# Optimization experiments

Hardware: AMD Instinct MI355X
Metric: run time of the kernel (lower is better)

The kernel has to match this reference:

```python
import jax, jax.numpy as jnp
import numpy as np

H = 2048          # hidden_size
F = 1408          # moe_intermediate_size
E = 64            # n_routed_experts
TOP_K = 6         # num_experts_per_tok
CAP = 512         # per-expert capacity (mean load ~192; overflow prob ~0)
SCALE = 1.0       # routed_scaling_factor
F_SH = 2 * F      # shared-expert intermediate (n_shared_experts=2)
B, S = 1, 2048


def setup_inputs() -> dict:
    key = jax.random.key(0)
    ks = jax.random.split(key, 8)
    s = 0.02
    return {
        "hidden_states": jax.random.normal(ks[0], (B, S, H), jnp.float32),
        "gate_w":  jax.random.normal(ks[1], (E, H), jnp.float32) * s,
        "w_gate":  jax.random.normal(ks[2], (E, H, F), jnp.float32) * s,
        "w_up":    jax.random.normal(ks[3], (E, H, F), jnp.float32) * s,
        "w_down":  jax.random.normal(ks[4], (E, F, H), jnp.float32) * s,
        "sh_gate": jax.random.normal(ks[5], (F_SH, H), jnp.float32) * s,
        "sh_up":   jax.random.normal(ks[6], (F_SH, H), jnp.float32) * s,
        "sh_down": jax.random.normal(ks[7], (H, F_SH), jnp.float32) * s,
    }


def reference(hidden_states, gate_w, w_gate, w_up, w_down, sh_gate, sh_up, sh_down):
    b, s, _ = hidden_states.shape
    x = hidden_states.reshape(-1, H)                       # [T, H]
    T = x.shape[0]

    # ---- gate: fp32 logits -> softmax -> top-k, scaled ----
    logits = x.astype(jnp.float32) @ gate_w.astype(jnp.float32).T   # [T, E]
    scores = jax.nn.softmax(logits, axis=-1)
    topk_w, topk_idx = jax.lax.top_k(scores, TOP_K)        # [T, K] (order irrelevant: summed)
    topk_w = topk_w * SCALE

    # ---- dispatch: sort expanded tokens by expert, scatter into [E, CAP, H] ----
    eid = topk_idx.reshape(-1)                             # [T*K]
    x_exp = jnp.repeat(x, TOP_K, axis=0)                   # [T*K, H] (token t repeated K times)
    order = jnp.argsort(eid)                               # stable sort by expert id
    eid_s = eid[order]
    counts = jnp.bincount(eid, length=E)
    starts = jnp.cumsum(counts) - counts                   # exclusive prefix sums
    pos = jnp.arange(T * TOP_K) - starts[eid_s]            # slot within expert
    valid = pos < CAP
    pos_c = jnp.where(valid, pos, CAP)                     # overflow -> scratch slot CAP
    buf = jnp.zeros((E, CAP + 1, H), x.dtype).at[eid_s, pos_c].set(x_exp[order])

    # ---- grouped expert SwiGLU MLP (grouped GEMM as batched einsum) ----
    g = jax.nn.silu(jnp.einsum('ech,ehf->ecf', buf, w_gate))
    u = jnp.einsum('ech,ehf->ecf', buf, w_up)
    d = jnp.einsum('ecf,efh->ech', g * u, w_down)          # [E, CAP+1, H]

    # ---- combine: gather, unsort, weighted sum over top-k ----
    out_s = jnp.where(valid[:, None], d[eid_s, pos_c], 0.0)
    out_exp = jnp.zeros_like(out_s).at[order].set(out_s)   # reverse_shuffle
    y = jnp.einsum('tkh,tk->th', out_exp.reshape(T, TOP_K, H), topk_w)
    y = y.astype(x.dtype).reshape(b, s, H)

    # ---- shared experts residual (dense SwiGLU MLP on identity) ----
    gs = jax.nn.silu(hidden_states @ sh_gate.T)
    us = hidden_states @ sh_up.T
    y = y + (gs * us) @ sh_down.T
    return y
```

## Files before the change

kernel.cpp:

```cpp
#include <hip/hip_runtime.h>
#include <hip/hip_bf16.h>

#define H 2048
#define FDIM 1408
#define NE 64
#define CAP 512
#define NTOK 2048
#define FSH 2816

typedef float  f32x4  __attribute__((ext_vector_type(4)));
typedef short  s16x8  __attribute__((ext_vector_type(8)));
typedef unsigned short u16;
typedef u16    u16x4v __attribute__((ext_vector_type(4)));

__device__ __forceinline__ u16 f2bf(float f) {
    union { float f; unsigned u; } v; v.f = f;
    unsigned u = v.u;
    u += 0x7fffu + ((u >> 16) & 1u);
    return (u16)(u >> 16);
}
__device__ __forceinline__ float bf2f(u16 b) {
    union { unsigned u; float f; } v; v.u = ((unsigned)b) << 16;
    return v.f;
}

#define BAR() do { asm volatile("s_waitcnt lgkmcnt(0)" ::: "memory"); \
                   __builtin_amdgcn_s_barrier(); } while (0)

__global__ __launch_bounds__(256) void xcvt(const float* __restrict__ x, u16* __restrict__ xb) {
    int i = blockIdx.x * 256 + threadIdx.x;
    const float4 a = ((const float4*)x)[2 * i];
    const float4 b = ((const float4*)x)[2 * i + 1];
    u16 v[8] = { f2bf(a.x), f2bf(a.y), f2bf(a.z), f2bf(a.w),
                 f2bf(b.x), f2bf(b.y), f2bf(b.z), f2bf(b.w) };
    *(s16x8*)(xb + (size_t)i * 8) = *(s16x8*)v;
}

__global__ void init_cnt(int* __restrict__ c) { c[threadIdx.x] = 0; }

__global__ __launch_bounds__(64) void gate_topk(
    const float* __restrict__ xg, const float* __restrict__ gw,
    int* __restrict__ cnt, int* __restrict__ tok_of,
    int* __restrict__ slot_enc, float* __restrict__ tw)
{
    const int t = blockIdx.x;
    const int lane = threadIdx.x;
    __shared__ float4 xs[512];
    const float4* xr = (const float4*)(xg + (size_t)t * H);
    #pragma unroll
    for (int i = 0; i < 8; ++i) xs[i * 64 + lane] = xr[i * 64 + lane];
    __syncthreads();

    const float4* gr = (const float4*)(gw + (size_t)lane * H);
    float acc = 0.f;
    #pragma unroll 4
    for (int i = 0; i < 512; ++i) {
        float4 a = xs[i], b = gr[i];
        acc += a.x * b.x + a.y * b.y + a.z * b.z + a.w * b.w;
    }
    float m = acc;
    #pragma unroll
    for (int off = 32; off; off >>= 1) m = fmaxf(m, __shfl_xor(m, off));
    float p = __expf(acc - m);
    float s = p;
    #pragma unroll
    for (int off = 32; off; off >>= 1) s += __shfl_xor(s, off);
    p = p / s;

    float myw = 0.f; int mye = 0;
    float v = p;
    for (int k = 0; k < 6; ++k) {
        float bv = v; int bi = lane;
        #pragma unroll
        for (int off = 32; off; off >>= 1) {
            float ov = __shfl_xor(bv, off);
            int   oi = __shfl_xor(bi, off);
            if (ov > bv || (ov == bv && oi < bi)) { bv = ov; bi = oi; }
        }
        if (lane == k)  { myw = bv; mye = bi; }
        if (lane == bi) v = -1.f;
    }
    if (lane < 6) {
        int slot = atomicAdd(&cnt[mye], 1);
        int enc = -1;
        if (slot < CAP) { tok_of[mye * CAP + slot] = t; enc = mye * CAP + slot; }
        slot_enc[t * 6 + lane] = enc;
        tw[t * 6 + lane] = myw;
    }
}

template<bool ROUTED>
__global__ __launch_bounds__(256, 2) void dual_gemm(
    const u16* __restrict__ xbf, const int* __restrict__ tok_of,
    const int* __restrict__ cnt_arr, const float* __restrict__ wg,
    const float* __restrict__ wu, u16* __restrict__ act, int Fd)
{
    __shared__ u16 As[2][8][256][8];
    __shared__ u16 Bs[2][2][8][32][8];

    int e = 0, cnt, m0, f0;
    if constexpr (ROUTED) {
        e = blockIdx.z;
        cnt = cnt_arr[e]; cnt = cnt < CAP ? cnt : CAP;
        f0 = blockIdx.x * 32; m0 = blockIdx.y * 256;
        if (m0 >= cnt) return;
    } else {
        cnt = NTOK;
        m0 = blockIdx.x * 256; f0 = blockIdx.y * 32;
    }

    const float* wg_e = wg;
    const float* wu_e = wu;
    u16* act_e = act;
    if constexpr (ROUTED) {
        wg_e += (size_t)e * H * Fd;
        wu_e += (size_t)e * H * Fd;
        act_e += (size_t)e * CAP * Fd;
    }

    const int tid = threadIdx.x;
    const int lane = tid & 63;
    const int wv = tid >> 6;

    const u16* aptr;
    {
        int srow = m0 + tid;
        if constexpr (ROUTED) {
            const int* tok = tok_of + e * CAP;
            aptr = xbf + (size_t)tok[srow < cnt ? srow : 0] * H;
        } else {
            aptr = xbf + (size_t)srow * H;
        }
    }
    const int mat = tid >> 7;
    const int bb = tid & 127;
    const float* bsrc;
    int n4 = 0, kq = 0, br = 0, bc = 0;
    if constexpr (ROUTED) {
        n4 = bb & 7; kq = bb >> 3;
        bsrc = (mat ? wu_e : wg_e) + (size_t)(kq * 4) * Fd + f0 + n4 * 4;
    } else {
        br = bb >> 2; bc = bb & 3;
        bsrc = (mat ? wu_e : wg_e) + (size_t)(f0 + br) * H + bc * 16;
    }

    s16x8 aR[8];
    f32x4 bR[4];
    f32x4 accg[4][2], accu[4][2];
    const f32x4 zero4 = {0.f, 0.f, 0.f, 0.f};
    #pragma unroll
    for (int i = 0; i < 4; ++i)
        #pragma unroll
        for (int j = 0; j < 2; ++j) { accg[i][j] = zero4; accu[i][j] = zero4; }

    auto LOAD = [&](int kt) {
        #pragma unroll
        for (int q = 0; q < 8; ++q) aR[q] = *(const s16x8*)(aptr + kt * 64 + q * 8);
        if constexpr (ROUTED) {
            #pragma unroll
            for (int j = 0; j < 4; ++j)
                bR[j] = *(const f32x4*)(bsrc + ((size_t)kt * 64 + j) * Fd);
        } else {
            #pragma unroll
            for (int q = 0; q < 4; ++q)
                bR[q] = *(const f32x4*)(bsrc + kt * 64 + q * 4);
        }
    };
    auto STORE = [&](int b) {
        #pragma unroll
        for (int q = 0; q < 8; ++q) *(s16x8*)&As[b][q][tid][0] = aR[q];
        if constexpr (ROUTED) {
            const int k8 = kq >> 1, ko = (kq & 1) * 4;
            #pragma unroll
            for (int c = 0; c < 4; ++c) {
                u16x4v v; v[0] = f2bf(bR[0][c]); v[1] = f2bf(bR[1][c]);
                          v[2] = f2bf(bR[2][c]); v[3] = f2bf(bR[3][c]);
                *(u16x4v*)&Bs[b][mat][k8][(n4 * 4 + c) ^ k8][ko] = v;
            }
        } else {
            #pragma unroll
            for (int h = 0; h < 2; ++h) {
                const int k8 = bc * 2 + h;
                u16 v[8];
                f32x4 x0 = bR[h * 2], x1 = bR[h * 2 + 1];
                v[0]=f2bf(x0[0]); v[1]=f2bf(x0[1]); v[2]=f2bf(x0[2]); v[3]=f2bf(x0[3]);
                v[4]=f2bf(x1[0]); v[5]=f2bf(x1[1]); v[6]=f2bf(x1[2]); v[7]=f2bf(x1[3]);
                *(s16x8*)&Bs[b][mat][k8][br ^ k8][0] = *(s16x8*)v;
            }
        }
    };

    LOAD(0); STORE(0); LOAD(1);
    BAR();
    for (int kt = 0; kt < H / 64; ++kt) {
        const int b = kt & 1;
        if (kt + 1 < H / 64) STORE(b ^ 1);
        if (kt + 2 < H / 64) LOAD(kt + 2);
        __builtin_amdgcn_s_setprio(1);
        #pragma unroll
        for (int kk = 0; kk < 2; ++kk) {
            const int k8 = kk * 4 + (lane >> 4);
            s16x8 a[4], bg[2], bu[2];
            #pragma unroll
            for (int mi = 0; mi < 4; ++mi)
                a[mi] = *(const s16x8*)&As[b][k8][wv * 64 + mi * 16 + (lane & 15)][0];
            #pragma unroll
            for (int ni = 0; ni < 2; ++ni) {
                const int np = (ni * 16 + (lane & 15)) ^ k8;
                bg[ni] = *(const s16x8*)&Bs[b][0][k8][np][0];
                bu[ni] = *(const s16x8*)&Bs[b][1][k8][np][0];
            }
            #pragma unroll
            for (int mi = 0; mi < 4; ++mi)
                #pragma unroll
                for (int ni = 0; ni < 2; ++ni) {
                    accg[mi][ni] = __builtin_amdgcn_mfma_f32_16x16x32_bf16(a[mi], bg[ni], accg[mi][ni], 0, 0, 0);
                    accu[mi][ni] = __builtin_amdgcn_mfma_f32_16x16x32_bf16(a[mi], bu[ni], accu[mi][ni], 0, 0, 0);
                }
        }
        __builtin_amdgcn_s_setprio(0);
        BAR();
    }

    #pragma unroll
    for (int mi = 0; mi < 4; ++mi)
        #pragma unroll
        for (int ni = 0; ni < 2; ++ni)
            #pragma unroll
            for (int r = 0; r < 4; ++r) {
                int srow = m0 + wv * 64 + mi * 16 + (lane >> 4) * 4 + r;
                if (srow < cnt) {
                    int fc = f0 + ni * 16 + (lane & 15);
                    float g = accg[mi][ni][r], u = accu[mi][ni][r];
                    float aa = (g / (1.f + __expf(-g))) * u;
                    act_e[(size_t)srow * Fd + fc] = f2bf(aa);
                }
            }
}

template<bool ROUTED>
__global__ __launch_bounds__(256, 2) void down_gemm(
    const u16* __restrict__ actA, const float* __restrict__ wdn,
    void* __restrict__ outp, const int* __restrict__ cnt_arr, int Kd)
{
    __shared__ u16 As[2][8][256][8];
    __shared__ u16 Bs[2][8][64][8];

    int e = 0, cnt, m0, n0;
    if constexpr (ROUTED) {
        e = blockIdx.z;
        cnt = cnt_arr[e]; cnt = cnt < CAP ? cnt : CAP;
        n0 = blockIdx.x * 64; m0 = blockIdx.y * 256;
        if (m0 >= cnt) return;
    } else {
        cnt = NTOK;
        m0 = blockIdx.x * 256; n0 = blockIdx.y * 64;
    }

    const u16* A_e = actA;
    const float* B_e = wdn;
    if constexpr (ROUTED) {
        A_e += (size_t)e * CAP * Kd;
        B_e += (size_t)e * Kd * H;
    }
    const int NT = Kd / 64;
    const int tid = threadIdx.x, lane = tid & 63, wv = tid >> 6;

    const u16* aptr;
    {
        int row = m0 + tid;
        if constexpr (ROUTED) aptr = A_e + (size_t)(row < cnt ? row : m0) * Kd;
        else aptr = A_e + (size_t)row * Kd;
    }
    const float* bsrc;
    int n4 = 0, kq = 0, br = 0, bc = 0;
    if constexpr (ROUTED) {
        n4 = tid & 15; kq = tid >> 4;
        bsrc = B_e + (size_t)(kq * 4) * H + n0 + n4 * 4;
    } else {
        br = tid >> 2; bc = tid & 3;
        bsrc = B_e + (size_t)(n0 + br) * FSH + bc * 16;
    }

    s16x8 aR[8];
    f32x4 bR[4];
    f32x4 acc[4][4];
    const f32x4 zero4 = {0.f, 0.f, 0.f, 0.f};
    #pragma unroll
    for (int i = 0; i < 4; ++i)
        #pragma unroll
        for (int j = 0; j < 4; ++j) acc[i][j] = zero4;

    auto LOAD = [&](int kt) {
        #pragma unroll
        for (int q = 0; q < 8; ++q) aR[q] = *(const s16x8*)(aptr + kt * 64 + q * 8);
        if constexpr (ROUTED) {
            #pragma unroll
            for (int j = 0; j < 4; ++j)
                bR[j] = *(const f32x4*)(bsrc + ((size_t)kt * 64 + j) * H);
        } else {
            #pragma unroll
            for (int q = 0; q < 4; ++q)
                bR[q] = *(const f32x4*)(bsrc + kt * 64 + q * 4);
        }
    };
    auto STORE = [&](int b) {
        #pragma unroll
        for (int q = 0; q < 8; ++q) *(s16x8*)&As[b][q][tid][0] = aR[q];
        if constexpr (ROUTED) {
            const int k8 = kq >> 1, ko = (kq & 1) * 4;
            #pragma unroll
            for (int c = 0; c < 4; ++c) {
                u16x4v v; v[0] = f2bf(bR[0][c]); v[1] = f2bf(bR[1][c]);
                          v[2] = f2bf(bR[2][c]); v[3] = f2bf(bR[3][c]);
                *(u16x4v*)&Bs[b][k8][(n4 * 4 + c) ^ k8][ko] = v;
            }
        } else {
            #pragma unroll
            for (int h = 0; h < 2; ++h) {
                const int k8 = bc * 2 + h;
                u16 v[8];
                f32x4 x0 = bR[h * 2], x1 = bR[h * 2 + 1];
                v[0]=f2bf(x0[0]); v[1]=f2bf(x0[1]); v[2]=f2bf(x0[2]); v[3]=f2bf(x0[3]);
                v[4]=f2bf(x1[0]); v[5]=f2bf(x1[1]); v[6]=f2bf(x1[2]); v[7]=f2bf(x1[3]);
                *(s16x8*)&Bs[b][k8][br ^ k8][0] = *(s16x8*)v;
            }
        }
    };

    LOAD(0); STORE(0); LOAD(1);
    BAR();
    for (int kt = 0; kt < NT; ++kt) {
        const int b = kt & 1;
        if (kt + 1 < NT) STORE(b ^ 1);
        if (kt + 2 < NT) LOAD(kt + 2);
        __builtin_amdgcn_s_setprio(1);
        #pragma unroll
        for (int kk = 0; kk < 2; ++kk) {
            const int k8 = kk * 4 + (lane >> 4);
            s16x8 a[4], bf[4];
            #pragma unroll
            for (int mi = 0; mi < 4; ++mi)
                a[mi] = *(const s16x8*)&As[b][k8][wv * 64 + mi * 16 + (lane & 15)][0];
            #pragma unroll
            for (int ni = 0; ni < 4; ++ni)
                bf[ni] = *(const s16x8*)&Bs[b][k8][(ni * 16 + (lane & 15)) ^ k8][0];
            #pragma unroll
            for (int mi = 0; mi < 4; ++mi)
                #pragma unroll
                for (int ni = 0; ni < 4; ++ni)
                    acc[mi][ni] = __builtin_amdgcn_mfma_f32_16x16x32_bf16(a[mi], bf[ni], acc[mi][ni], 0, 0, 0);
        }
        __builtin_amdgcn_s_setprio(0);
        BAR();
    }

    #pragma unroll
    for (int mi = 0; mi < 4; ++mi)
        #pragma unroll
        for (int ni = 0; ni < 4; ++ni)
            #pragma unroll
            for (int r = 0; r < 4; ++r) {
                int srow = m0 + wv * 64 + mi * 16 + (lane >> 4) * 4 + r;
                if (srow < cnt) {
                    int col = n0 + ni * 16 + (lane & 15);
                    float vv = acc[mi][ni][r];
                    if constexpr (ROUTED)
                        ((u16*)outp)[(size_t)e * CAP * H + (size_t)srow * H + col] = f2bf(vv);
                    else
                        ((float*)outp)[(size_t)srow * H + col] = vv;
                }
            }
}

__global__ __launch_bounds__(256) void combine(
    float* __restrict__ y, const u16* __restrict__ d,
    const int* __restrict__ slot_enc, const float* __restrict__ tw)
{
    const int t = blockIdx.x, tid = threadIdx.x;
    int enc[6]; float w[6];
    #pragma unroll
    for (int k = 0; k < 6; ++k) {
        enc[k] = slot_enc[t * 6 + k];
        w[k] = tw[t * 6 + k];
    }
    float4* yrow = (float4*)(y + (size_t)t * H);
    #pragma unroll
    for (int it = 0; it < 2; ++it) {
        int h4 = it * 256 + tid;
        float4 acc = yrow[h4];
        #pragma unroll
        for (int k = 0; k < 6; ++k) {
            if (enc[k] >= 0) {
                ushort4 dv = ((const ushort4*)(d + (size_t)enc[k] * H))[h4];
                acc.x += w[k] * bf2f(dv.x);
                acc.y += w[k] * bf2f(dv.y);
                acc.z += w[k] * bf2f(dv.z);
                acc.w += w[k] * bf2f(dv.w);
            }
        }
        yrow[h4] = acc;
    }
}

extern "C" void kernel_launch(void* const* d_in, const int* in_sizes, int n_in,
                              void* d_out, int out_size, void* d_ws, size_t ws_size,
                              hipStream_t stream) {
    const float* x       = (const float*)d_in[0];
    const float* gw      = (const float*)d_in[1];
    const float* w_gate  = (const float*)d_in[2];
    const float* w_up    = (const float*)d_in[3];
    const float* w_down  = (const float*)d_in[4];
    const float* sh_gate = (const float*)d_in[5];
    const float* sh_up   = (const float*)d_in[6];
    const float* sh_down = (const float*)d_in[7];
    float* y = (float*)d_out;

    char* wsb = (char*)d_ws;
    int*   cnt      = (int*)(wsb + 0);
    int*   tok_of   = (int*)(wsb + 512);
    int*   slot_enc = (int*)(wsb + 512 + 131072);
    float* tw       = (float*)(wsb + 512 + 131072 + 49152);
    u16*   act      = (u16*)(wsb + 230144);
    u16*   actsh    = (u16*)(wsb + 230144 + 92274688);
    u16*   dbuf     = (u16*)(wsb + 230144 + 92274688 + 11534336);
    u16*   xbf      = dbuf;

    init_cnt<<<1, 64, 0, stream>>>(cnt);
    xcvt<<<NTOK * H / 8 / 256, 256, 0, stream>>>(x, xbf);
    gate_topk<<<NTOK, 64, 0, stream>>>(x, gw, cnt, tok_of, slot_enc, tw);
    dual_gemm<true><<<dim3(FDIM / 32, 2, NE), 256, 0, stream>>>(
        xbf, tok_of, cnt, w_gate, w_up, act, FDIM);
    dual_gemm<false><<<dim3(NTOK / 256, FSH / 32, 1), 256, 0, stream>>>(
        xbf, nullptr, nullptr, sh_gate, sh_up, actsh, FSH);
    down_gemm<true><<<dim3(H / 64, 2, NE), 256, 0, stream>>>(
        act, w_down, (void*)dbuf, cnt, FDIM);
    down_gemm<false><<<dim3(NTOK / 256, H / 64, 1), 256, 0, stream>>>(
        actsh, sh_down, (void*)y, nullptr, FSH);
    combine<<<NTOK, 256, 0, stream>>>(y, dbuf, slot_enc, tw);
}
```

Baseline: 1.107 ms.

## Load A tiles straight into LDS and double-buffer B weight registers

In both the gate/up and down-projection GEMM kernels, the bf16 A tile is now copied from global memory directly into LDS with global_load_lds, so it no longer passes through VGPRs and explicit LDS stores. The fp32 B weights are held in two alternating register buffers. They are converted and written to LDS after the MFMA block, and explicit vmcnt waits plus scheduling fences control the overlap. The goal is to cut register pressure and VALU/LDS store traffic and to hide global latency behind compute. The risks are that the hand-counted vmcnt values must match the issue order exactly, and that the down kernel now reads unclamped padding rows of the expert buffer.

Result: slower. 1.465 ms (+32.4%).

```diff
diff --git a/kernel.cpp b/kernel.cpp
--- a/kernel.cpp
+++ b/kernel.cpp
@@ -23,9 +23,15 @@
     union { unsigned u; float f; } v; v.u = ((unsigned)b) << 16;
     return v.f;
 }
-
-#define BAR() do { asm volatile("s_waitcnt lgkmcnt(0)" ::: "memory"); \
-                   __builtin_amdgcn_s_barrier(); } while (0)
+__device__ __forceinline__ void glds16(const u16* g, u16* l) {
+    __builtin_amdgcn_global_load_lds(
+        (const __attribute__((address_space(1))) unsigned int*)g,
+        (__attribute__((address_space(3))) unsigned int*)l, 16, 0, 0);
+}
+
+#define WAIT_VM(N)  asm volatile("s_waitcnt vmcnt(" #N ")" ::: "memory")
+#define WAIT_LGKM() asm volatile("s_waitcnt lgkmcnt(0)" ::: "memory")
+#define SCHED_FENCE() __builtin_amdgcn_sched_barrier(0)
 
 __global__ __launch_bounds__(256) void xcvt(const float* __restrict__ x, u16* __restrict__ xb) {
     int i = blockIdx.x * 256 + threadIdx.x;
@@ -121,6 +127,7 @@
     const int tid = threadIdx.x;
     const int lane = tid & 63;
     const int wv = tid >> 6;
+    const int NT = H / 64;
 
     const u16* aptr;
     {
@@ -144,8 +151,7 @@
         bsrc = (mat ? wu_e : wg_e) + (size_t)(f0 + br) * H + bc * 16;
     }
 
-    s16x8 aR[8];
-    f32x4 bR[4];
+    f32x4 bRa[4], bRb[4];
     f32x4 accg[4][2], accu[4][2];
     const f32x4 zero4 = {0.f, 0.f, 0.f, 0.f};
     #pragma unroll
@@ -153,28 +159,29 @@
         #pragma unroll
         for (int j = 0; j < 2; ++j) { accg[i][j] = zero4; accu[i][j] = zero4; }
 
-    auto LOAD = [&](int kt) {
-        #pragma unroll
-        for (int q = 0; q < 8; ++q) aR[q] = *(const s16x8*)(aptr + kt * 64 + q * 8);
+    auto GLDS_A = [&](int kt, int b) {
+        #pragma unroll
+        for (int q = 0; q < 8; ++q)
+            glds16(aptr + kt * 64 + q * 8, &As[b][q][wv * 64][0]);
+    };
+    auto LOADB = [&](int kt, f32x4 (&dst)[4]) {
         if constexpr (ROUTED) {
             #pragma unroll
             for (int j = 0; j < 4; ++j)
-                bR[j] = *(const f32x4*)(bsrc + ((size_t)kt * 64 + j) * Fd);
+                dst[j] = *(const f32x4*)(bsrc + ((size_t)kt * 64 + j) * Fd);
         } else {
             #pragma unroll
             for (int q = 0; q < 4; ++q)
-                bR[q] = *(const f32x4*)(bsrc + kt * 64 + q * 4);
-        }
-    };
-    auto STORE = [&](int b) {
-        #pragma unroll
-        for (int q = 0; q < 8; ++q) *(s16x8*)&As[b][q][tid][0] = aR[q];
+                dst[q] = *(const f32x4*)(bsrc + kt * 64 + q * 4);
+        }
+    };
+    auto STOREB = [&](const f32x4 (&src)[4], int b) {
         if constexpr (ROUTED) {
             const int k8 = kq >> 1, ko = (kq & 1) * 4;
             #pragma unroll
             for (int c = 0; c < 4; ++c) {
-                u16x4v v; v[0] = f2bf(bR[0][c]); v[1] = f2bf(bR[1][c]);
-                          v[2] = f2bf(bR[2][c]); v[3] = f2bf(bR[3][c]);
+                u16x4v v; v[0] = f2bf(src[0][c]); v[1] = f2bf(src[1][c]);
+                          v[2] = f2bf(src[2][c]); v[3] = f2bf(src[3][c]);
                 *(u16x4v*)&Bs[b][mat][k8][(n4 * 4 + c) ^ k8][ko] = v;
             }
         } else {
@@ -182,20 +189,14 @@
             for (int h = 0; h < 2; ++h) {
                 const int k8 = bc * 2 + h;
                 u16 v[8];
-                f32x4 x0 = bR[h * 2], x1 = bR[h * 2 + 1];
+                f32x4 x0 = src[h * 2], x1 = src[h * 2 + 1];
                 v[0]=f2bf(x0[0]); v[1]=f2bf(x0[1]); v[2]=f2bf(x0[2]); v[3]=f2bf(x0[3]);
                 v[4]=f2bf(x1[0]); v[5]=f2bf(x1[1]); v[6]=f2bf(x1[2]); v[7]=f2bf(x1[3]);
                 *(s16x8*)&Bs[b][mat][k8][br ^ k8][0] = *(s16x8*)v;
             }
         }
     };
-
-    LOAD(0); STORE(0); LOAD(1);
-    BAR();
-    for (int kt = 0; kt < H / 64; ++kt) {
-        const int b = kt & 1;
-        if (kt + 1 < H / 64) STORE(b ^ 1);
-        if (kt + 2 < H / 64) LOAD(kt + 2);
+    auto COMPUTE = [&](int b) {
         __builtin_amdgcn_s_setprio(1);
         #pragma unroll
         for (int kk = 0; kk < 2; ++kk) {
@@ -219,7 +220,33 @@
                 }
         }
         __builtin_amdgcn_s_setprio(0);
-        BAR();
+    };
+
+    GLDS_A(0, 0);            SCHED_FENCE();
+    LOADB(0, bRa);           SCHED_FENCE();
+    LOADB(1, bRb);           SCHED_FENCE();
+    WAIT_VM(4);
+    STOREB(bRa, 0);
+    WAIT_LGKM();
+    __builtin_amdgcn_s_barrier();
+    SCHED_FENCE();
+
+    for (int kt = 0; kt < NT; ++kt) {
+        const int b = kt & 1;
+        if (kt + 1 < NT) GLDS_A(kt + 1, b ^ 1);
+        SCHED_FENCE();
+        if ((kt & 1) == 0) { if (kt + 2 < NT) LOADB(kt + 2, bRa); }
+        else               { if (kt + 2 < NT) LOADB(kt + 2, bRb); }
+        SCHED_FENCE();
+        COMPUTE(b);
+        if (kt + 1 < NT) {
+            if ((kt & 1) == 0) STOREB(bRb, b ^ 1);
+            else               STOREB(bRa, b ^ 1);
+        }
+        if (kt + 2 < NT) { WAIT_VM(4); } else { WAIT_VM(0); }
+        WAIT_LGKM();
+        __builtin_amdgcn_s_barrier();
+        SCHED_FENCE();
     }
 
     #pragma unroll
@@ -266,24 +293,19 @@
     const int NT = Kd / 64;
     const int tid = threadIdx.x, lane = tid & 63, wv = tid >> 6;
 
-    const u16* aptr;
-    {
-        int row = m0 + tid;
-        if constexpr (ROUTED) aptr = A_e + (size_t)(row < cnt ? row : m0) * Kd;
-        else aptr = A_e + (size_t)row * Kd;
-    }
+    const u16* aptr = A_e + (size_t)(m0 + tid) * Kd;
+
     const float* bsrc;
-    int n4 = 0, kq = 0, br = 0, bc = 0;
+    int n4 = 0, kq = 0, dr = 0, dc = 0;
     if constexpr (ROUTED) {
         n4 = tid & 15; kq = tid >> 4;
         bsrc = B_e + (size_t)(kq * 4) * H + n0 + n4 * 4;
     } else {
-        br = tid >> 2; bc = tid & 3;
-        bsrc = B_e + (size_t)(n0 + br) * FSH + bc * 16;
-    }
-
-    s16x8 aR[8];
-    f32x4 bR[4];
+        dr = tid >> 2; dc = tid & 3;
+        bsrc = B_e + (size_t)(n0 + dr) * FSH + dc * 16;
+    }
+
+    f32x4 bRa[4], bRb[4];
     f32x4 acc[4][4];
     const f32x4 zero4 = {0.f, 0.f, 0.f, 0.f};
     #pragma unroll
@@ -291,49 +313,44 @@
         #pragma unroll
         for (int j = 0; j < 4; ++j) acc[i][j] = zero4;
 
-    auto LOAD = [&](int kt) {
-        #pragma unroll
-        for (int q = 0; q < 8; ++q) aR[q] = *(const s16x8*)(aptr + kt * 64 + q * 8);
+    auto GLDS_A = [&](int kt, int b) {
+        #pragma unroll
+        for (int q = 0; q < 8; ++q)
+            glds16(aptr + kt * 64 + q * 8, &As[b][q][wv * 64][0]);
+    };
+    auto LOADB = [&](int kt, f32x4 (&dst)[4]) {
         if constexpr (ROUTED) {
             #pragma unroll
             for (int j = 0; j < 4; ++j)
-                bR[j] = *(const f32x4*)(bsrc + ((size_t)kt * 64 + j) * H);
+                dst[j] = *(const f32x4*)(bsrc + ((size_t)kt * 64 + j) * H);
         } else {
             #pragma unroll
             for (int q = 0; q < 4; ++q)
-                bR[q] = *(const f32x4*)(bsrc + kt * 64 + q * 4);
-        }
-    };
-    auto STORE = [&](int b) {
-        #pragma unroll
-        for (int q = 0; q < 8; ++q) *(s16x8*)&As[b][q][tid][0] = aR[q];
+                dst[q] = *(const f32x4*)(bsrc + kt * 64 + q * 4);
+        }
+    };
+    auto STOREB = [&](const f32x4 (&src)[4], int b) {
         if constexpr (ROUTED) {
             const int k8 = kq >> 1, ko = (kq & 1) * 4;
             #pragma unroll
             for (int c = 0; c < 4; ++c) {
-                u16x4v v; v[0] = f2bf(bR[0][c]); v[1] = f2bf(bR[1][c]);
-                          v[2] = f2bf(bR[2][c]); v[3] = f2bf(bR[3][c]);
+                u16x4v v; v[0] = f2bf(src[0][c]); v[1] = f2bf(src[1][c]);
+                          v[2] = f2bf(src[2][c]); v[3] = f2bf(src[3][c]);
                 *(u16x4v*)&Bs[b][k8][(n4 * 4 + c) ^ k8][ko] = v;
             }
         } else {
             #pragma unroll
             for (int h = 0; h < 2; ++h) {
-                const int k8 = bc * 2 + h;
+                const int k8 = dc * 2 + h;
                 u16 v[8];
-                f32x4 x0 = bR[h * 2], x1 = bR[h * 2 + 1];
+                f32x4 x0 = src[h * 2], x1 = src[h * 2 + 1];
                 v[0]=f2bf(x0[0]); v[1]=f2bf(x0[1]); v[2]=f2bf(x0[2]); v[3]=f2bf(x0[3]);
                 v[4]=f2bf(x1[0]); v[5]=f2bf(x1[1]); v[6]=f2bf(x1[2]); v[7]=f2bf(x1[3]);
-                *(s16x8*)&Bs[b][k8][br ^ k8][0] = *(s16x8*)v;
-            }
-        }
-    };
-
-    LOAD(0); STORE(0); LOAD(1);
-    BAR();
-    for (int kt = 0; kt < NT; ++kt) {
-        const int b = kt & 1;
-        if (kt + 1 < NT) STORE(b ^ 1);
-        if (kt + 2 < NT) LOAD(kt + 2);
+                *(s16x8*)&Bs[b][k8][dr ^ k8][0] = *(s16x8*)v;
+            }
+        }
+    };
+    auto COMPUTE = [&](int b) {
         __builtin_amdgcn_s_setprio(1);
         #pragma unroll
         for (int kk = 0; kk < 2; ++kk) {
@@ -352,7 +369,33 @@
                     acc[mi][ni] = __builtin_amdgcn_mfma_f32_16x16x32_bf16(a[mi], bf[ni], acc[mi][ni], 0, 0, 0);
         }
         __builtin_amdgcn_s_setprio(0);
-        BAR();
+    };
+
+    GLDS_A(0, 0);            SCHED_FENCE();
+    LOADB(0, bRa);           SCHED_FENCE();
+    LOADB(1, bRb);           SCHED_FENCE();
+    WAIT_VM(4);
+    STOREB(bRa, 0);
+    WAIT_LGKM();
+    __builtin_amdgcn_s_barrier();
+    SCHED_FENCE();
+
+    for (int kt = 0; kt < NT; ++kt) {
+        const int b = kt & 1;
+        if (kt + 1 < NT) GLDS_A(kt + 1, b ^ 1);
+        SCHED_FENCE();
+        if ((kt & 1) == 0) { if (kt + 2 < NT) LOADB(kt + 2, bRa); }
+        else               { if (kt + 2 < NT) LOADB(kt + 2, bRb); }
+        SCHED_FENCE();
+        COMPUTE(b);
+        if (kt + 1 < NT) {
+            if ((kt & 1) == 0) STOREB(bRb, b ^ 1);
+            else               STOREB(bRa, b ^ 1);
+        }
+        if (kt + 2 < NT) { WAIT_VM(4); } else { WAIT_VM(0); }
+        WAIT_LGKM();
+        __builtin_amdgcn_s_barrier();
+        SCHED_FENCE();
     }
 
     #pragma unroll
```

## Deepen GEMM prefetch to two register stages with XOR-swizzled LDS tiles

Applied to the files above, without the earlier changes.

Both the dual gate/up GEMM and the down GEMM now keep two register sets of global loads in flight. The k-loop is unrolled by two so that tile kt+3 is loaded while tile kt is computed, and scheduling fences keep the compiler from reordering across these stages. The LDS layout changes from a k8-major layout to row-major 64-wide rows with an XOR swizzle, and A-tile loads now read coalesced row chunks with eight rows per thread. This is meant to hide global-memory latency and cut LDS bank conflicts, at the cost of more registers, which may hurt occupancy under launch_bounds(256,2).

New measurement: 1.328 ms. 20.0% more time.

```diff
diff --git a/kernel.cpp b/kernel.cpp
--- a/kernel.cpp
+++ b/kernel.cpp
@@ -23,9 +23,17 @@
     union { unsigned u; float f; } v; v.u = ((unsigned)b) << 16;
     return v.f;
 }
+__device__ __forceinline__ int swze(int row) {
+    return (((row & 7) ^ ((row >> 3) & 7)) << 3);
+}
+__device__ __forceinline__ void wr4(u16* dst, float a, float b, float c, float d) {
+    u16x4v v; v[0] = f2bf(a); v[1] = f2bf(b); v[2] = f2bf(c); v[3] = f2bf(d);
+    *(u16x4v*)dst = v;
+}
 
 #define BAR() do { asm volatile("s_waitcnt lgkmcnt(0)" ::: "memory"); \
                    __builtin_amdgcn_s_barrier(); } while (0)
+#define SCHED_FENCE() __builtin_amdgcn_sched_barrier(0)
 
 __global__ __launch_bounds__(256) void xcvt(const float* __restrict__ x, u16* __restrict__ xb) {
     int i = blockIdx.x * 256 + threadIdx.x;
@@ -95,8 +103,9 @@
     const int* __restrict__ cnt_arr, const float* __restrict__ wg,
     const float* __restrict__ wu, u16* __restrict__ act, int Fd)
 {
-    __shared__ u16 As[2][8][256][8];
-    __shared__ u16 Bs[2][2][8][32][8];
+    __shared__ u16 As[2][256 * 64];
+    __shared__ u16 Bgs[2][32 * 64];
+    __shared__ u16 Bus[2][32 * 64];
 
     int e = 0, cnt, m0, f0;
     if constexpr (ROUTED) {
@@ -121,31 +130,35 @@
     const int tid = threadIdx.x;
     const int lane = tid & 63;
     const int wv = tid >> 6;
-
-    const u16* aptr;
-    {
-        int srow = m0 + tid;
+    const int NT = H / 64;
+
+    const int ac = tid & 7;
+    int arl[8];
+    const u16* arow[8];
+    #pragma unroll
+    for (int it = 0; it < 8; ++it) {
+        int row = it * 32 + (tid >> 3);
+        arl[it] = row;
+        int srow = m0 + row;
         if constexpr (ROUTED) {
             const int* tok = tok_of + e * CAP;
-            aptr = xbf + (size_t)tok[srow < cnt ? srow : 0] * H;
+            arow[it] = xbf + (size_t)tok[srow < cnt ? srow : 0] * H;
         } else {
-            aptr = xbf + (size_t)srow * H;
+            arow[it] = xbf + (size_t)srow * H;
         }
     }
     const int mat = tid >> 7;
     const int bb = tid & 127;
     const float* bsrc;
-    int n4 = 0, kq = 0, br = 0, bc = 0;
-    if constexpr (ROUTED) {
-        n4 = bb & 7; kq = bb >> 3;
-        bsrc = (mat ? wu_e : wg_e) + (size_t)(kq * 4) * Fd + f0 + n4 * 4;
+    int bn4 = 0, bkb = 0, br = 0, bc = 0;
+    if constexpr (ROUTED) {
+        bn4 = bb & 7; bkb = bb >> 3;
+        bsrc = (mat ? wu_e : wg_e) + (size_t)(bkb * 4) * Fd + f0 + bn4 * 4;
     } else {
         br = bb >> 2; bc = bb & 3;
         bsrc = (mat ? wu_e : wg_e) + (size_t)(f0 + br) * H + bc * 16;
     }
 
-    s16x8 aR[8];
-    f32x4 bR[4];
     f32x4 accg[4][2], accu[4][2];
     const f32x4 zero4 = {0.f, 0.f, 0.f, 0.f};
     #pragma unroll
@@ -153,62 +166,60 @@
         #pragma unroll
         for (int j = 0; j < 2; ++j) { accg[i][j] = zero4; accu[i][j] = zero4; }
 
-    auto LOAD = [&](int kt) {
-        #pragma unroll
-        for (int q = 0; q < 8; ++q) aR[q] = *(const s16x8*)(aptr + kt * 64 + q * 8);
+    s16x8 aR0[8], aR1[8];
+    f32x4 bR0[4], bR1[4];
+
+    auto LOADA = [&](int kt, s16x8 (&ar)[8]) {
+        #pragma unroll
+        for (int it = 0; it < 8; ++it)
+            ar[it] = *(const s16x8*)(arow[it] + kt * 64 + ac * 8);
+    };
+    auto LOADB = [&](int kt, f32x4 (&brg)[4]) {
         if constexpr (ROUTED) {
             #pragma unroll
             for (int j = 0; j < 4; ++j)
-                bR[j] = *(const f32x4*)(bsrc + ((size_t)kt * 64 + j) * Fd);
+                brg[j] = *(const f32x4*)(bsrc + ((size_t)kt * 64 + j) * Fd);
         } else {
             #pragma unroll
             for (int q = 0; q < 4; ++q)
-                bR[q] = *(const f32x4*)(bsrc + kt * 64 + q * 4);
-        }
-    };
-    auto STORE = [&](int b) {
-        #pragma unroll
-        for (int q = 0; q < 8; ++q) *(s16x8*)&As[b][q][tid][0] = aR[q];
+                brg[q] = *(const f32x4*)(bsrc + kt * 64 + q * 4);
+        }
+    };
+    auto STORE = [&](const s16x8 (&ar)[8], const f32x4 (&brg)[4], int b) {
+        #pragma unroll
+        for (int it = 0; it < 8; ++it)
+            *(s16x8*)&As[b][arl[it] * 64 + ((ac * 8) ^ swze(arl[it]))] = ar[it];
+        u16* Bdst = mat ? Bus[b] : Bgs[b];
         if constexpr (ROUTED) {
-            const int k8 = kq >> 1, ko = (kq & 1) * 4;
-            #pragma unroll
-            for (int c = 0; c < 4; ++c) {
-                u16x4v v; v[0] = f2bf(bR[0][c]); v[1] = f2bf(bR[1][c]);
-                          v[2] = f2bf(bR[2][c]); v[3] = f2bf(bR[3][c]);
-                *(u16x4v*)&Bs[b][mat][k8][(n4 * 4 + c) ^ k8][ko] = v;
+            #pragma unroll
+            for (int j = 0; j < 4; ++j) {
+                int rr = bn4 * 4 + j;
+                wr4(&Bdst[rr * 64 + ((bkb * 4) ^ swze(rr))],
+                    brg[0][j], brg[1][j], brg[2][j], brg[3][j]);
             }
         } else {
             #pragma unroll
-            for (int h = 0; h < 2; ++h) {
-                const int k8 = bc * 2 + h;
-                u16 v[8];
-                f32x4 x0 = bR[h * 2], x1 = bR[h * 2 + 1];
-                v[0]=f2bf(x0[0]); v[1]=f2bf(x0[1]); v[2]=f2bf(x0[2]); v[3]=f2bf(x0[3]);
-                v[4]=f2bf(x1[0]); v[5]=f2bf(x1[1]); v[6]=f2bf(x1[2]); v[7]=f2bf(x1[3]);
-                *(s16x8*)&Bs[b][mat][k8][br ^ k8][0] = *(s16x8*)v;
-            }
-        }
-    };
-
-    LOAD(0); STORE(0); LOAD(1);
-    BAR();
-    for (int kt = 0; kt < H / 64; ++kt) {
-        const int b = kt & 1;
-        if (kt + 1 < H / 64) STORE(b ^ 1);
-        if (kt + 2 < H / 64) LOAD(kt + 2);
+            for (int q = 0; q < 4; ++q)
+                wr4(&Bdst[br * 64 + (((bc * 16 + q * 4)) ^ swze(br))],
+                    brg[q].x, brg[q].y, brg[q].z, brg[q].w);
+        }
+    };
+    auto COMPUTE = [&](int b) {
         __builtin_amdgcn_s_setprio(1);
         #pragma unroll
         for (int kk = 0; kk < 2; ++kk) {
-            const int k8 = kk * 4 + (lane >> 4);
+            const int ko = kk * 32 + (lane >> 4) * 8;
             s16x8 a[4], bg[2], bu[2];
             #pragma unroll
-            for (int mi = 0; mi < 4; ++mi)
-                a[mi] = *(const s16x8*)&As[b][k8][wv * 64 + mi * 16 + (lane & 15)][0];
+            for (int mi = 0; mi < 4; ++mi) {
+                int r = wv * 64 + mi * 16 + (lane & 15);
+                a[mi] = *(const s16x8*)&As[b][r * 64 + (ko ^ swze(r))];
+            }
             #pragma unroll
             for (int ni = 0; ni < 2; ++ni) {
-                const int np = (ni * 16 + (lane & 15)) ^ k8;
-                bg[ni] = *(const s16x8*)&Bs[b][0][k8][np][0];
-                bu[ni] = *(const s16x8*)&Bs[b][1][k8][np][0];
+                int r = ni * 16 + (lane & 15);
+                bg[ni] = *(const s16x8*)&Bgs[b][r * 64 + (ko ^ swze(r))];
+                bu[ni] = *(const s16x8*)&Bus[b][r * 64 + (ko ^ swze(r))];
             }
             #pragma unroll
             for (int mi = 0; mi < 4; ++mi)
@@ -219,7 +230,27 @@
                 }
         }
         __builtin_amdgcn_s_setprio(0);
-        BAR();
+    };
+
+    LOADB(0, bR0); LOADA(0, aR0);
+    LOADB(1, bR1); LOADA(1, aR1);
+    STORE(aR0, bR0, 0);
+    LOADB(2, bR0); LOADA(2, aR0);
+    BAR(); SCHED_FENCE();
+
+    for (int kt = 0; kt < NT; kt += 2) {
+        STORE(aR1, bR1, 1);
+        if (kt + 3 < NT) { LOADB(kt + 3, bR1); LOADA(kt + 3, aR1); }
+        SCHED_FENCE();
+        COMPUTE(0);
+        BAR(); SCHED_FENCE();
+        if (kt + 2 < NT) {
+            STORE(aR0, bR0, 0);
+            if (kt + 4 < NT) { LOADB(kt + 4, bR0); LOADA(kt + 4, aR0); }
+        }
+        SCHED_FENCE();
+        COMPUTE(1);
+        BAR(); SCHED_FENCE();
     }
 
     #pragma unroll
@@ -243,8 +274,8 @@
     const u16* __restrict__ actA, const float* __restrict__ wdn,
     void* __restrict__ outp, const int* __restrict__ cnt_arr, int Kd)
 {
-    __shared__ u16 As[2][8][256][8];
-    __shared__ u16 Bs[2][8][64][8];
+    __shared__ u16 As[2][256 * 64];
+    __shared__ u16 Bs[2][64 * 64];
 
     int e = 0, cnt, m0, n0;
     if constexpr (ROUTED) {
@@ -266,24 +297,25 @@
     const int NT = Kd / 64;
     const int tid = threadIdx.x, lane = tid & 63, wv = tid >> 6;
 
-    const u16* aptr;
-    {
-        int row = m0 + tid;
-        if constexpr (ROUTED) aptr = A_e + (size_t)(row < cnt ? row : m0) * Kd;
-        else aptr = A_e + (size_t)row * Kd;
+    const int ac = tid & 7;
+    int arl[8];
+    const u16* arow[8];
+    #pragma unroll
+    for (int it = 0; it < 8; ++it) {
+        int row = it * 32 + (tid >> 3);
+        arl[it] = row;
+        arow[it] = A_e + (size_t)(m0 + row) * Kd;
     }
     const float* bsrc;
-    int n4 = 0, kq = 0, br = 0, bc = 0;
-    if constexpr (ROUTED) {
-        n4 = tid & 15; kq = tid >> 4;
-        bsrc = B_e + (size_t)(kq * 4) * H + n0 + n4 * 4;
+    int bn4 = 0, bkq = 0, dr = 0, dc = 0;
+    if constexpr (ROUTED) {
+        bn4 = tid & 15; bkq = tid >> 4;
+        bsrc = B_e + (size_t)(bkq * 4) * H + n0 + bn4 * 4;
     } else {
-        br = tid >> 2; bc = tid & 3;
-        bsrc = B_e + (size_t)(n0 + br) * FSH + bc * 16;
-    }
-
-    s16x8 aR[8];
-    f32x4 bR[4];
+        dr = tid >> 2; dc = tid & 3;
+        bsrc = B_e + (size_t)(n0 + dr) * FSH + dc * 16;
+    }
+
     f32x4 acc[4][4];
     const f32x4 zero4 = {0.f, 0.f, 0.f, 0.f};
     #pragma unroll
@@ -291,60 +323,59 @@
         #pragma unroll
         for (int j = 0; j < 4; ++j) acc[i][j] = zero4;
 
-    auto LOAD = [&](int kt) {
-        #pragma unroll
-        for (int q = 0; q < 8; ++q) aR[q] = *(const s16x8*)(aptr + kt * 64 + q * 8);
+    s16x8 aR0[8], aR1[8];
+    f32x4 bR0[4], bR1[4];
+
+    auto LOADA = [&](int kt, s16x8 (&ar)[8]) {
+        #pragma unroll
+        for (int it = 0; it < 8; ++it)
+            ar[it] = *(const s16x8*)(arow[it] + kt * 64 + ac * 8);
+    };
+    auto LOADB = [&](int kt, f32x4 (&brg)[4]) {
         if constexpr (ROUTED) {
             #pragma unroll
             for (int j = 0; j < 4; ++j)
-                bR[j] = *(const f32x4*)(bsrc + ((size_t)kt * 64 + j) * H);
+                brg[j] = *(const f32x4*)(bsrc + ((size_t)kt * 64 + j) * H);
         } else {
             #pragma unroll
             for (int q = 0; q < 4; ++q)
-                bR[q] = *(const f32x4*)(bsrc + kt * 64 + q * 4);
-        }
-    };
-    auto STORE = [&](int b) {
-        #pragma unroll
-        for (int q = 0; q < 8; ++q) *(s16x8*)&As[b][q][tid][0] = aR[q];
+                brg[q] = *(const f32x4*)(bsrc + kt * 64 + q * 4);
+        }
+    };
+    auto STORE = [&](const s16x8 (&ar)[8], const f32x4 (&brg)[4], int b) {
+        #pragma unroll
+        for (int it = 0; it < 8; ++it)
+            *(s16x8*)&As[b][arl[it] * 64 + ((ac * 8) ^ swze(arl[it]))] = ar[it];
         if constexpr (ROUTED) {
-            const int k8 = kq >> 1, ko = (kq & 1) * 4;
-            #pragma unroll
-            for (int c = 0; c < 4; ++c) {
-                u16x4v v; v[0] = f2bf(bR[0][c]); v[1] = f2bf(bR[1][c]);
-                          v[2] = f2bf(bR[2][c]); v[3] = f2bf(bR[3][c]);
-                *(u16x4v*)&Bs[b][k8][(n4 * 4 + c) ^ k8][ko] = v;
+            #pragma unroll
+            for (int j = 0; j < 4; ++j) {
+                int rr = bn4 * 4 + j;
+                wr4(&Bs[b][rr * 64 + ((bkq * 4) ^ swze(rr))],
+                    brg[0][j], brg[1][j], brg[2][j], brg[3][j]);
             }
         } else {
             #pragma unroll
-            for (int h = 0; h < 2; ++h) {
-                const int k8 = bc * 2 + h;
-                u16 v[8];
-                f32x4 x0 = bR[h * 2], x1 = bR[h * 2 + 1];
-                v[0]=f2bf(x0[0]); v[1]=f2bf(x0[1]); v[2]=f2bf(x0[2]); v[3]=f2bf(x0[3]);
-                v[4]=f2bf(x1[0]); v[5]=f2bf(x1[1]); v[6]=f2bf(x1[2]); v[7]=f2bf(x1[3]);
-                *(s16x8*)&Bs[b][k8][br ^ k8][0] = *(s16x8*)v;
-            }
-        }
-    };
-
-    LOAD(0); STORE(0); LOAD(1);
-    BAR();
-    for (int kt = 0; kt < NT; ++kt) {
-        const int b = kt & 1;
-        if (kt + 1 < NT) STORE(b ^ 1);
-        if (kt + 2 < NT) LOAD(kt + 2);
+            for (int q = 0; q < 4; ++q)
+                wr4(&Bs[b][dr * 64 + (((dc * 16 + q * 4)) ^ swze(dr))],
+                    brg[q].x, brg[q].y, brg[q].z, brg[q].w);
+        }
+    };
+    auto COMPUTE = [&](int b) {
         __builtin_amdgcn_s_setprio(1);
         #pragma unroll
         for (int kk = 0; kk < 2; ++kk) {
-            const int k8 = kk * 4 + (lane >> 4);
+            const int ko = kk * 32 + (lane >> 4) * 8;
             s16x8 a[4], bf[4];
             #pragma unroll
-            for (int mi = 0; mi < 4; ++mi)
-                a[mi] = *(const s16x8*)&As[b][k8][wv * 64 + mi * 16 + (lane & 15)][0];
-            #pragma unroll
-            for (int ni = 0; ni < 4; ++ni)
-                bf[ni] = *(const s16x8*)&Bs[b][k8][(ni * 16 + (lane & 15)) ^ k8][0];
+            for (int mi = 0; mi < 4; ++mi) {
+                int r = wv * 64 + mi * 16 + (lane & 15);
+                a[mi] = *(const s16x8*)&As[b][r * 64 + (ko ^ swze(r))];
+            }
+            #pragma unroll
+            for (int ni = 0; ni < 4; ++ni) {
+                int r = ni * 16 + (lane & 15);
+                bf[ni] = *(const s16x8*)&Bs[b][r * 64 + (ko ^ swze(r))];
+            }
             #pragma unroll
             for (int mi = 0; mi < 4; ++mi)
                 #pragma unroll
@@ -352,7 +383,27 @@
                     acc[mi][ni] = __builtin_amdgcn_mfma_f32_16x16x32_bf16(a[mi], bf[ni], acc[mi][ni], 0, 0, 0);
         }
         __builtin_amdgcn_s_setprio(0);
-        BAR();
+    };
+
+    LOADB(0, bR0); LOADA(0, aR0);
+    LOADB(1, bR1); LOADA(1, aR1);
+    STORE(aR0, bR0, 0);
+    LOADB(2, bR0); LOADA(2, aR0);
+    BAR(); SCHED_FENCE();
+
+    for (int kt = 0; kt < NT; kt += 2) {
+        STORE(aR1, bR1, 1);
+        if (kt + 3 < NT) { LOADB(kt + 3, bR1); LOADA(kt + 3, aR1); }
+        SCHED_FENCE();
+        COMPUTE(0);
+        BAR(); SCHED_FENCE();
+        if (kt + 2 < NT) {
+            STORE(aR0, bR0, 0);
+            if (kt + 4 < NT) { LOADB(kt + 4, bR0); LOADA(kt + 4, aR0); }
+        }
+        SCHED_FENCE();
+        COMPUTE(1);
+        BAR(); SCHED_FENCE();
     }
 
     #pragma unroll
```
